# Optimization experiments

Hardware: AMD Instinct MI355X
Metric: run time of the kernel (lower is better)

## Reference

```python
import jax, jax.numpy as jnp
import numpy as np

MAX_VAL = 10000.0
KS = (1, 5, 10, 20, 50)
B, V, L = 256, 128000, 200


def setup_inputs() -> dict:
    key = jax.random.key(0)
    k1, k2, k3 = jax.random.split(key, 3)
    scores = jax.random.normal(k1, (B, V), dtype=jnp.float32)
    labels = jax.random.randint(k2, (B,), 0, V, dtype=jnp.int64)
    seqs = jax.random.randint(k3, (B, L), 0, V, dtype=jnp.int64)
    return {"scores": scores, "labels": labels, "seqs": seqs}


def reference(scores, labels, seqs):
    b = scores.shape[0]
    rows = jnp.arange(b)
    # gather predicted score for the true label BEFORE masking (torch order)
    predicts = scores[rows, labels]  # [B]
    # scatter -MAX_VAL at history items (masked scatter)
    masked = scores.at[rows[:, None], seqs].set(-MAX_VAL)  # [B, V]
    valid_length = (masked > -MAX_VAL).sum(-1).astype(jnp.float32)  # [B]
    rank = (predicts[:, None] < masked).sum(-1).astype(jnp.float32)  # [B]
    res = []
    for k in KS:
        indicator = (rank < k).astype(jnp.float32)
        res.append((indicator / jnp.log2(rank + 2.0)).mean())  # NDCG@k
        res.append(indicator.mean())  # Recall@k
    res.append((1.0 / (rank + 1.0)).mean())  # MRR
    res.append((1.0 - rank / valid_length).mean())  # AUC-like
    res.append(jnp.float32(0.0))
    return jnp.stack(res)
```

## Files before the change

kernel.cpp:

```cpp
#include <hip/hip_runtime.h>
#include <math.h>

#define B_CONST 256
#define V_CONST 128000
#define L_CONST 200
#define SLICES  25


__global__ __launch_bounds__(256) void rank_count_kernel(
    const float* __restrict__ scores,
    const int* __restrict__ labels,
    const int* __restrict__ seqs,
    int* __restrict__ partial,
    int* __restrict__ sub,
    int* __restrict__ dist)
{
    const int slice = blockIdx.x;
    const int b     = blockIdx.y;
    const int tid   = threadIdx.x;

    const float* row = scores + (size_t)b * V_CONST;

    const float4* row4 = (const float4*)row;
    const int base = slice * 1280 + tid;
    float4 a0 = row4[base];
    float4 a1 = row4[base + 256];
    float4 a2 = row4[base + 512];
    float4 a3 = row4[base + 768];
    float4 a4 = row4[base + 1024];

    const float predict = row[labels[b]];

    __shared__ int s_cnt, s_sub, s_dist;
    __shared__ int s_seq[L_CONST];
    if (tid == 0) { s_cnt = 0; s_sub = 0; s_dist = 0; }
    if (slice == 0 && tid < L_CONST) s_seq[tid] = seqs[b * L_CONST + tid];
    __syncthreads();

    int cnt = 0;
    cnt += (a0.x > predict) + (a0.y > predict) + (a0.z > predict) + (a0.w > predict);
    cnt += (a1.x > predict) + (a1.y > predict) + (a1.z > predict) + (a1.w > predict);
    cnt += (a2.x > predict) + (a2.y > predict) + (a2.z > predict) + (a2.w > predict);
    cnt += (a3.x > predict) + (a3.y > predict) + (a3.z > predict) + (a3.w > predict);
    cnt += (a4.x > predict) + (a4.y > predict) + (a4.z > predict) + (a4.w > predict);

    #pragma unroll
    for (int off = 32; off > 0; off >>= 1)
        cnt += __shfl_down(cnt, off, 64);
    if ((tid & 63) == 0) atomicAdd(&s_cnt, cnt);

    if (slice == 0 && tid < L_CONST) {
        const int s = s_seq[tid];
        const float sv = row[s];
        bool first = true;
        for (int j = 0; j < tid; ++j) {
            if (s_seq[j] == s) { first = false; break; }
        }
        if (first) {
            atomicAdd(&s_dist, 1);
            if (sv > predict) atomicAdd(&s_sub, 1);
        }
    }
    __syncthreads();

    if (tid == 0) {
        partial[slice * B_CONST + b] = s_cnt;
        if (slice == 0) {
            sub[b]  = s_sub;
            dist[b] = s_dist;
        }
    }
}

__global__ __launch_bounds__(256) void finalize_kernel(
    const int* __restrict__ partial,
    const int* __restrict__ sub,
    const int* __restrict__ dist,
    float* __restrict__ out)
{
    const int b = threadIdx.x;
    int gt = 0;
    #pragma unroll
    for (int s = 0; s < SLICES; ++s) gt += partial[s * B_CONST + b];
    const float rank  = (float)(gt - sub[b]);
    const float valid = (float)(V_CONST - dist[b]);

    const float ks[5] = {1.0f, 5.0f, 10.0f, 20.0f, 50.0f};
    float vals[12];
    const float invlog = 1.0f / log2f(rank + 2.0f);
    #pragma unroll
    for (int i = 0; i < 5; ++i) {
        const float ind = (rank < ks[i]) ? 1.0f : 0.0f;
        vals[2 * i]     = ind * invlog;
        vals[2 * i + 1] = ind;
    }
    vals[10] = 1.0f / (rank + 1.0f);
    vals[11] = 1.0f - rank / valid;

    __shared__ float red[4];
    for (int q = 0; q < 12; ++q) {
        float v = vals[q];
        #pragma unroll
        for (int off = 32; off > 0; off >>= 1)
            v += __shfl_down(v, off, 64);
        if ((b & 63) == 0) red[b >> 6] = v;
        __syncthreads();
        if (b == 0) out[q] = (red[0] + red[1] + red[2] + red[3]) * (1.0f / B_CONST);
        __syncthreads();
    }
    if (b == 0) out[12] = 0.0f;
}

extern "C" void kernel_launch(void* const* d_in, const int* in_sizes, int n_in,
                              void* d_out, int out_size, void* d_ws, size_t ws_size,
                              hipStream_t stream) {
    const float* scores = (const float*)d_in[0];
    const int*   labels = (const int*)d_in[1];
    const int*   seqs   = (const int*)d_in[2];
    float* out = (float*)d_out;
    int*   ws  = (int*)d_ws;

    int* partial = ws;
    int* sub     = ws + SLICES * B_CONST;
    int* dist    = ws + SLICES * B_CONST + B_CONST;

    rank_count_kernel<<<dim3(SLICES, B_CONST), 256, 0, stream>>>(
        scores, labels, seqs, partial, sub, dist);
    finalize_kernel<<<1, 256, 0, stream>>>(partial, sub, dist, out);
}
```

Baseline: 200.0 us.

## Use nontemporal loads, replace LDS atomics with wave reductions, single-wave finalize

Score loads switch to nontemporal vector loads to avoid polluting cache with streamed data. Shared-memory atomics for counts are replaced by per-wave shuffle reductions written to small LDS arrays. The history-sequence gather is issued before the sync. The finalize kernel is shrunk to one wave that handles four rows per lane and skips the block-level barriers. The main kernel is bandwidth bound, so these mostly trim latency and small overheads.

```diff
diff --git a/kernel.cpp b/kernel.cpp
--- a/kernel.cpp
+++ b/kernel.cpp
@@ -5,6 +5,8 @@
 #define V_CONST 128000
 #define L_CONST 200
 #define SLICES  25
+
+typedef float f32x4 __attribute__((ext_vector_type(4)));
 
 
 __global__ __launch_bounds__(256) void rank_count_kernel(
@@ -18,97 +20,119 @@
     const int slice = blockIdx.x;
     const int b     = blockIdx.y;
     const int tid   = threadIdx.x;
+    const int wave  = tid >> 6;
 
     const float* row = scores + (size_t)b * V_CONST;
 
-    const float4* row4 = (const float4*)row;
+    const f32x4* row4 = (const f32x4*)row;
     const int base = slice * 1280 + tid;
-    float4 a0 = row4[base];
-    float4 a1 = row4[base + 256];
-    float4 a2 = row4[base + 512];
-    float4 a3 = row4[base + 768];
-    float4 a4 = row4[base + 1024];
+    f32x4 a0 = __builtin_nontemporal_load(row4 + base);
+    f32x4 a1 = __builtin_nontemporal_load(row4 + base + 256);
+    f32x4 a2 = __builtin_nontemporal_load(row4 + base + 512);
+    f32x4 a3 = __builtin_nontemporal_load(row4 + base + 768);
+    f32x4 a4 = __builtin_nontemporal_load(row4 + base + 1024);
 
     const float predict = row[labels[b]];
 
-    __shared__ int s_cnt, s_sub, s_dist;
     __shared__ int s_seq[L_CONST];
-    if (tid == 0) { s_cnt = 0; s_sub = 0; s_dist = 0; }
-    if (slice == 0 && tid < L_CONST) s_seq[tid] = seqs[b * L_CONST + tid];
-    __syncthreads();
+    __shared__ int s_wcnt[4];
+    __shared__ int s_wsub[4];
+    __shared__ int s_wdist[4];
+
+    int myseq = 0;
+    float sv = 0.0f;
+    if (slice == 0 && tid < L_CONST) {
+        myseq = seqs[b * L_CONST + tid];
+        s_seq[tid] = myseq;
+        sv = row[myseq];
+    }
 
     int cnt = 0;
-    cnt += (a0.x > predict) + (a0.y > predict) + (a0.z > predict) + (a0.w > predict);
-    cnt += (a1.x > predict) + (a1.y > predict) + (a1.z > predict) + (a1.w > predict);
-    cnt += (a2.x > predict) + (a2.y > predict) + (a2.z > predict) + (a2.w > predict);
-    cnt += (a3.x > predict) + (a3.y > predict) + (a3.z > predict) + (a3.w > predict);
-    cnt += (a4.x > predict) + (a4.y > predict) + (a4.z > predict) + (a4.w > predict);
+    cnt += (a0[0] > predict) + (a0[1] > predict) + (a0[2] > predict) + (a0[3] > predict);
+    cnt += (a1[0] > predict) + (a1[1] > predict) + (a1[2] > predict) + (a1[3] > predict);
+    cnt += (a2[0] > predict) + (a2[1] > predict) + (a2[2] > predict) + (a2[3] > predict);
+    cnt += (a3[0] > predict) + (a3[1] > predict) + (a3[2] > predict) + (a3[3] > predict);
+    cnt += (a4[0] > predict) + (a4[1] > predict) + (a4[2] > predict) + (a4[3] > predict);
 
     #pragma unroll
     for (int off = 32; off > 0; off >>= 1)
         cnt += __shfl_down(cnt, off, 64);
-    if ((tid & 63) == 0) atomicAdd(&s_cnt, cnt);
+    if ((tid & 63) == 0) s_wcnt[wave] = cnt;
 
-    if (slice == 0 && tid < L_CONST) {
-        const int s = s_seq[tid];
-        const float sv = row[s];
-        bool first = true;
-        for (int j = 0; j < tid; ++j) {
-            if (s_seq[j] == s) { first = false; break; }
+    __syncthreads();
+
+    if (slice == 0) {
+        int idist = 0, isub = 0;
+        if (tid < L_CONST) {
+            bool first = true;
+            for (int j = 0; j < tid; ++j) {
+                if (s_seq[j] == myseq) { first = false; break; }
+            }
+            if (first) {
+                idist = 1;
+                if (sv > predict) isub = 1;
+            }
         }
-        if (first) {
-            atomicAdd(&s_dist, 1);
-            if (sv > predict) atomicAdd(&s_sub, 1);
+        #pragma unroll
+        for (int off = 32; off > 0; off >>= 1) {
+            idist += __shfl_down(idist, off, 64);
+            isub  += __shfl_down(isub,  off, 64);
+        }
+        if ((tid & 63) == 0) { s_wsub[wave] = isub; s_wdist[wave] = idist; }
+        __syncthreads();
+        if (tid == 0) {
+            sub[b]  = s_wsub[0] + s_wsub[1] + s_wsub[2] + s_wsub[3];
+            dist[b] = s_wdist[0] + s_wdist[1] + s_wdist[2] + s_wdist[3];
         }
     }
-    __syncthreads();
 
-    if (tid == 0) {
-        partial[slice * B_CONST + b] = s_cnt;
-        if (slice == 0) {
-            sub[b]  = s_sub;
-            dist[b] = s_dist;
-        }
-    }
+    if (tid == 0)
+        partial[slice * B_CONST + b] = s_wcnt[0] + s_wcnt[1] + s_wcnt[2] + s_wcnt[3];
 }
 
-__global__ __launch_bounds__(256) void finalize_kernel(
+__global__ __launch_bounds__(64) void finalize_kernel(
     const int* __restrict__ partial,
     const int* __restrict__ sub,
     const int* __restrict__ dist,
     float* __restrict__ out)
 {
-    const int b = threadIdx.x;
-    int gt = 0;
+    const int l = threadIdx.x;
+
+    float acc[12];
     #pragma unroll
-    for (int s = 0; s < SLICES; ++s) gt += partial[s * B_CONST + b];
-    const float rank  = (float)(gt - sub[b]);
-    const float valid = (float)(V_CONST - dist[b]);
+    for (int q = 0; q < 12; ++q) acc[q] = 0.0f;
 
     const float ks[5] = {1.0f, 5.0f, 10.0f, 20.0f, 50.0f};
-    float vals[12];
-    const float invlog = 1.0f / log2f(rank + 2.0f);
+
     #pragma unroll
-    for (int i = 0; i < 5; ++i) {
-        const float ind = (rank < ks[i]) ? 1.0f : 0.0f;
-        vals[2 * i]     = ind * invlog;
-        vals[2 * i + 1] = ind;
+    for (int r = 0; r < 4; ++r) {
+        const int b = l + 64 * r;
+        int gt = 0;
+        #pragma unroll
+        for (int s = 0; s < SLICES; ++s) gt += partial[s * B_CONST + b];
+        const float rank  = (float)(gt - sub[b]);
+        const float valid = (float)(V_CONST - dist[b]);
+
+        const float invlog = 1.0f / log2f(rank + 2.0f);
+        #pragma unroll
+        for (int i = 0; i < 5; ++i) {
+            const float ind = (rank < ks[i]) ? 1.0f : 0.0f;
+            acc[2 * i]     += ind * invlog;
+            acc[2 * i + 1] += ind;
+        }
+        acc[10] += 1.0f / (rank + 1.0f);
+        acc[11] += 1.0f - rank / valid;
     }
-    vals[10] = 1.0f / (rank + 1.0f);
-    vals[11] = 1.0f - rank / valid;
 
-    __shared__ float red[4];
+    #pragma unroll
     for (int q = 0; q < 12; ++q) {
-        float v = vals[q];
+        float v = acc[q];
         #pragma unroll
         for (int off = 32; off > 0; off >>= 1)
             v += __shfl_down(v, off, 64);
-        if ((b & 63) == 0) red[b >> 6] = v;
-        __syncthreads();
-        if (b == 0) out[q] = (red[0] + red[1] + red[2] + red[3]) * (1.0f / B_CONST);
-        __syncthreads();
+        if (l == 0) out[q] = v * (1.0f / B_CONST);
     }
-    if (b == 0) out[12] = 0.0f;
+    if (l == 0) out[12] = 0.0f;
 }
 
 extern "C" void kernel_launch(void* const* d_in, const int* in_sizes, int n_in,
@@ -126,5 +150,5 @@
 
     rank_count_kernel<<<dim3(SLICES, B_CONST), 256, 0, stream>>>(
         scores, labels, seqs, partial, sub, dist);
-    finalize_kernel<<<1, 256, 0, stream>>>(partial, sub, dist, out);
+    finalize_kernel<<<1, 64, 0, stream>>>(partial, sub, dist, out);
 }
```

Result: no change. 198.1 us (-0.9%).
